# Kernel tuning notes

Hardware: AMD Instinct MI355X
Metric: run time of the kernel (lower is better)

## Reference

```python
import jax, jax.numpy as jnp
import numpy as np

N_FEAT = 1024
N_HIDDEN = 31


def _lstm_cell(x, h, c, W_ih, W_hh, b_ih, b_hh):
    # PyTorch LSTMCell: gates ordered i, f, g, o
    gates = x @ W_ih.T + b_ih + h @ W_hh.T + b_hh
    i, f, g, o = jnp.split(gates, 4, axis=-1)
    i = jax.nn.sigmoid(i)
    f = jax.nn.sigmoid(f)
    g = jnp.tanh(g)
    o = jax.nn.sigmoid(o)
    c_new = f * c + i * g
    h_new = o * jnp.tanh(c_new)
    return h_new, c_new


def setup_inputs() -> dict:
    key = jax.random.key(0)
    ks = jax.random.split(key, 12)
    B, T = 64, 512
    s1 = 1.0 / np.sqrt(N_HIDDEN)
    inp = {
        "input": jax.random.normal(ks[0], (B, T, N_FEAT), dtype=jnp.float32),
        "W_ih1": jax.random.uniform(ks[1], (4 * N_HIDDEN, N_FEAT), jnp.float32, -s1, s1),
        "W_hh1": jax.random.uniform(ks[2], (4 * N_HIDDEN, N_HIDDEN), jnp.float32, -s1, s1),
        "b_ih1": jax.random.uniform(ks[3], (4 * N_HIDDEN,), jnp.float32, -s1, s1),
        "b_hh1": jax.random.uniform(ks[4], (4 * N_HIDDEN,), jnp.float32, -s1, s1),
        "W_ih2": jax.random.uniform(ks[5], (4 * N_HIDDEN, N_HIDDEN), jnp.float32, -s1, s1),
        "W_hh2": jax.random.uniform(ks[6], (4 * N_HIDDEN, N_HIDDEN), jnp.float32, -s1, s1),
        "b_ih2": jax.random.uniform(ks[7], (4 * N_HIDDEN,), jnp.float32, -s1, s1),
        "b_hh2": jax.random.uniform(ks[8], (4 * N_HIDDEN,), jnp.float32, -s1, s1),
        "W_lin": jax.random.uniform(ks[9], (N_FEAT, N_HIDDEN), jnp.float32, -s1, s1),
        "b_lin": jax.random.uniform(ks[10], (N_FEAT,), jnp.float32, -s1, s1),
        "future": 16,
    }
    return inp


def reference(input, W_ih1, W_hh1, b_ih1, b_hh1, W_ih2, W_hh2, b_ih2, b_hh2, W_lin, b_lin, future):
    B = input.shape[0]
    h0 = jnp.zeros((B, N_HIDDEN), dtype=input.dtype)
    state0 = (h0, h0, h0, h0)  # h_t, c_t, h_t2, c_t2

    def step(state, x_t):
        h_t, c_t, h_t2, c_t2 = state
        h_t, c_t = _lstm_cell(x_t, h_t, c_t, W_ih1, W_hh1, b_ih1, b_hh1)
        h_t2, c_t2 = _lstm_cell(h_t, h_t2, c_t2, W_ih2, W_hh2, b_ih2, b_hh2)
        out = h_t2 @ W_lin.T + b_lin  # [B, N_FEAT]
        return (h_t, c_t, h_t2, c_t2), out

    # teacher-forced pass over the given sequence
    xs = jnp.swapaxes(input, 0, 1)  # [T, B, F]
    state, outs = jax.lax.scan(step, state0, xs)
    last = outs[-1]

    def fut_step(carry, _):
        state, out = carry
        state, out = step(state, out)
        return (state, out), out

    if future > 0:
        _, fut_outs = jax.lax.scan(fut_step, (state, last), None, length=future)
        outs = jnp.concatenate([outs, fut_outs], axis=0)

    return jnp.swapaxes(outs, 0, 1)  # [B, T+future, N_FEAT]
```

## Files before the change

kernel.cpp:

```cpp
#include <hip/hip_runtime.h>
#include <hip/hip_bf16.h>

#define BB_  64
#define TT_  512
#define FF_  1024
#define HH_  31
#define GG_  124
#define FUT_ 16
#define TTOT_ 528
#define OUT_ROW_ ((size_t)TTOT_ * FF_)

#define PRE1_OFF ((size_t)0)
#define H2A_OFF  (PRE1_OFF + (size_t)TT_*64*128)
#define WT_OFF   (H2A_OFF  + (size_t)TTOT_*64*32)
#define MV_OFF   (WT_OFF   + 31*1024)

__device__ __forceinline__ float rdlane(float v, int k) {
    return __uint_as_float(__builtin_amdgcn_readlane(__float_as_uint(v), k));
}

#define REP31(M) M(0) M(1) M(2) M(3) M(4) M(5) M(6) M(7) M(8) M(9) \
                 M(10) M(11) M(12) M(13) M(14) M(15) M(16) M(17) M(18) M(19) \
                 M(20) M(21) M(22) M(23) M(24) M(25) M(26) M(27) M(28) M(29) M(30)

__global__ void k0_prep(const float* __restrict__ Wlin, float* __restrict__ WT) {
    int i = blockIdx.x * 256 + threadIdx.x;
    int j = i / 31;
    int k = i - j * 31;
    WT[k * 1024 + j] = Wlin[i];
}

__global__ __launch_bounds__(64) void k0b_mv(
    const float* __restrict__ Wih1, const float* __restrict__ Wlin,
    const float* __restrict__ blin, float* __restrict__ Mv)
{
    int i = blockIdx.x * 64 + threadIdx.x;
    int g = i >> 5, k = i & 31;
    const float* wr = Wih1 + (size_t)g * FF_;
    float acc = 0.0f;
    if (k < 31) {
#pragma unroll 8
        for (int j = 0; j < FF_; j++) acc += wr[j] * Wlin[j * 31 + k];
    } else {
#pragma unroll 8
        for (int j = 0; j < FF_; j++) acc += wr[j] * blin[j];
    }
    Mv[i] = acc;
}

__global__ __launch_bounds__(256) void k1_pregate(
    const float* __restrict__ X,
    const float* __restrict__ Wih1,
    const float* __restrict__ bih1,
    const float* __restrict__ bhh1,
    float* __restrict__ pre1)
{
    __shared__ __align__(16) float xs[32][64];
    __shared__ __align__(16) float ws[32][128];
    const int tid  = threadIdx.x;
    const int t    = blockIdx.x;
    const int tcol = tid & 31, trow = tid >> 5;
    const int c0 = tcol * 4, r0 = trow * 8;

    float4 acc[8];
#pragma unroll
    for (int r = 0; r < 8; r++) acc[r] = make_float4(0.f, 0.f, 0.f, 0.f);

    for (int kc = 0; kc < 32; ++kc) {
        const int k0 = kc * 32;
#pragma unroll
        for (int p = 0; p < 2; p++) {
            int i = tid + p * 256;
            int r = i >> 3, f = i & 7;
            float4 v = *(const float4*)(X + (size_t)r * TT_ * FF_ + (size_t)t * FF_ + k0 + f * 4);
            xs[f * 4 + 0][r] = v.x; xs[f * 4 + 1][r] = v.y;
            xs[f * 4 + 2][r] = v.z; xs[f * 4 + 3][r] = v.w;
        }
#pragma unroll
        for (int p = 0; p < 4; p++) {
            int i = tid + p * 256;
            int g = i >> 3, f = i & 7;
            float4 v = make_float4(0.f, 0.f, 0.f, 0.f);
            if (g < GG_) v = *(const float4*)(Wih1 + (size_t)g * FF_ + k0 + f * 4);
            ws[f * 4 + 0][g] = v.x; ws[f * 4 + 1][g] = v.y;
            ws[f * 4 + 2][g] = v.z; ws[f * 4 + 3][g] = v.w;
        }
        __syncthreads();
#pragma unroll
        for (int k = 0; k < 32; k++) {
            float4 wv = *(const float4*)&ws[k][c0];
            float4 xa = *(const float4*)&xs[k][r0];
            float4 xb = *(const float4*)&xs[k][r0 + 4];
            float rx[8] = {xa.x, xa.y, xa.z, xa.w, xb.x, xb.y, xb.z, xb.w};
#pragma unroll
            for (int r = 0; r < 8; r++) {
                acc[r].x += rx[r] * wv.x; acc[r].y += rx[r] * wv.y;
                acc[r].z += rx[r] * wv.z; acc[r].w += rx[r] * wv.w;
            }
        }
        __syncthreads();
    }
    float bias[4];
#pragma unroll
    for (int cc = 0; cc < 4; cc++) {
        int c = c0 + cc;
        bias[cc] = (c < GG_) ? (bih1[c] + bhh1[c]) : 0.0f;
    }
#pragma unroll
    for (int r = 0; r < 8; r++) {
        int m = t * 64 + r0 + r;
        float4 o = acc[r];
        o.x += bias[0]; o.y += bias[1]; o.z += bias[2]; o.w += bias[3];
        *(float4*)(pre1 + (size_t)m * 128 + c0) = o;
    }
}

__global__ __attribute__((amdgpu_flat_work_group_size(128, 128), amdgpu_waves_per_eu(1)))
void k2_recur(
    const float* __restrict__ pre1,
    const float* __restrict__ Whh1,
    const float* __restrict__ Wih2,
    const float* __restrict__ Whh2,
    const float* __restrict__ bih1, const float* __restrict__ bhh1,
    const float* __restrict__ bih2, const float* __restrict__ bhh2,
    const float* __restrict__ Mv,
    float* __restrict__ h2a)
{
    __shared__ float gA[2][128];
    __shared__ float g2[2][128];
    const int L  = threadIdx.x;
    const int bb = blockIdx.x;
    const int j  = L & 63;
    const int gc = (L < GG_) ? L : (GG_ - 1);
    const bool isg = (gc >= 62 && gc < 93);
    const bool own = (j < HH_);

#define WLOAD(k) float w1_##k  = Whh1[gc * 31 + k]; \
                 float wi2_##k = Wih2[gc * 31 + k]; \
                 float wh2_##k = Whh2[gc * 31 + k];
    REP31(WLOAD)
#undef WLOAD
#define WPIN(k) asm("" : "+v"(w1_##k), "+v"(wi2_##k), "+v"(wh2_##k));
    REP31(WPIN)
#undef WPIN

    const float b2c = bih2[gc] + bhh2[gc];

    float hv1 = 0.0f, cv1 = 0.0f, hv2 = 0.0f, cv2 = 0.0f;

    float cur0 = pre1[(size_t)bb * 128 + L];
    float pnxt = pre1[((size_t)1 * 64 + bb) * 128 + L];
    {
        float a = cur0;
#define DOTP(k) { float hk = rdlane(hv1, k); a += w1_##k * hk; }
        REP31(DOTP)
#undef DOTP
        float z = isg ? (2.0f * a) : a;
        float s = 1.0f / (1.0f + __expf(-z));
        gA[1][L] = isg ? (2.0f * s - 1.0f) : s;
    }
    __syncthreads();
    if (own) {
        float ig = gA[1][j];
        float fg = gA[1][j + 31];
        float gg = gA[1][j + 62];
        float og = gA[1][j + 93];
        cv1 = fg * cv1 + ig * gg;
        float e = __expf(-2.0f * cv1);
        hv1 = og * (2.0f / (1.0f + e) - 1.0f);
    }

    for (int t = 0; t < TT_ - 1; t++) {
        const int pb = t & 1;
        const float cur = pnxt;
        float pld = 0.0f;
        if (t + 2 < TT_) pld = pre1[((size_t)(t + 2) * 64 + bb) * 128 + L];

        float b = b2c;
        float a = cur;
#define DOTM(k) { float h1k = rdlane(hv1, k); float h2k = rdlane(hv2, k); \
                  b += wi2_##k * h1k + wh2_##k * h2k; \
                  a += w1_##k * h1k; }
        REP31(DOTM)
#undef DOTM
        {
            float z = isg ? (2.0f * b) : b;
            float s = 1.0f / (1.0f + __expf(-z));
            g2[pb][L] = isg ? (2.0f * s - 1.0f) : s;
        }
        {
            float z = isg ? (2.0f * a) : a;
            float s = 1.0f / (1.0f + __expf(-z));
            gA[pb][L] = isg ? (2.0f * s - 1.0f) : s;
        }
        __syncthreads();
        if (own) {
            float ig = g2[pb][j];
            float fg = g2[pb][j + 31];
            float gg = g2[pb][j + 62];
            float og = g2[pb][j + 93];
            cv2 = fg * cv2 + ig * gg;
            float e = __expf(-2.0f * cv2);
            hv2 = og * (2.0f / (1.0f + e) - 1.0f);
            float i1 = gA[pb][j];
            float f1 = gA[pb][j + 31];
            float g1v = gA[pb][j + 62];
            float o1 = gA[pb][j + 93];
            cv1 = f1 * cv1 + i1 * g1v;
            float e1 = __expf(-2.0f * cv1);
            hv1 = o1 * (2.0f / (1.0f + e1) - 1.0f);
        }
        if (L < HH_) h2a[((size_t)t * 64 + bb) * 32 + L] = hv2;
        pnxt = pld;
    }

    {
        float b = b2c;
#define DOTT(k) { float h1k = rdlane(hv1, k); float h2k = rdlane(hv2, k); \
                  b += wi2_##k * h1k + wh2_##k * h2k; }
        REP31(DOTT)
#undef DOTT
        float z = isg ? (2.0f * b) : b;
        float s = 1.0f / (1.0f + __expf(-z));
        g2[1][L] = isg ? (2.0f * s - 1.0f) : s;
    }
    __syncthreads();
    if (own) {
        float ig = g2[1][j];
        float fg = g2[1][j + 31];
        float gg = g2[1][j + 62];
        float og = g2[1][j + 93];
        cv2 = fg * cv2 + ig * gg;
        float e = __expf(-2.0f * cv2);
        hv2 = og * (2.0f / (1.0f + e) - 1.0f);
    }
    if (L < HH_) h2a[((size_t)(TT_ - 1) * 64 + bb) * 32 + L] = hv2;

#define MLOAD(k) float m_##k = Mv[gc * 32 + k];
    REP31(MLOAD)
#undef MLOAD
    float m_31 = Mv[gc * 32 + 31];
#define MPIN(k) asm("" : "+v"(m_##k));
    REP31(MPIN)
#undef MPIN
    asm("" : "+v"(m_31));
    const float b1c = bih1[gc] + bhh1[gc];

    for (int sft = 0; sft < FUT_; sft++) {
        float a = b1c + m_31;
#define DOTF1(k) { float h2k = rdlane(hv2, k); a += m_##k * h2k; }
        REP31(DOTF1)
#undef DOTF1
#define DOTF2(k) { float hk = rdlane(hv1, k); a += w1_##k * hk; }
        REP31(DOTF2)
#undef DOTF2
        {
            float z = isg ? (2.0f * a) : a;
            float s = 1.0f / (1.0f + __expf(-z));
            gA[0][L] = isg ? (2.0f * s - 1.0f) : s;
        }
        __syncthreads();
        if (own) {
            float ig = gA[0][j];
            float fg = gA[0][j + 31];
            float gg = gA[0][j + 62];
            float og = gA[0][j + 93];
            cv1 = fg * cv1 + ig * gg;
            float e = __expf(-2.0f * cv1);
            hv1 = og * (2.0f / (1.0f + e) - 1.0f);
        }
        float b = b2c;
#define DOTF3(k) { float h1k = rdlane(hv1, k); float h2k = rdlane(hv2, k); \
                   b += wi2_##k * h1k + wh2_##k * h2k; }
        REP31(DOTF3)
#undef DOTF3
        {
            float z = isg ? (2.0f * b) : b;
            float s = 1.0f / (1.0f + __expf(-z));
            g2[0][L] = isg ? (2.0f * s - 1.0f) : s;
        }
        __syncthreads();
        if (own) {
            float ig = g2[0][j];
            float fg = g2[0][j + 31];
            float gg = g2[0][j + 62];
            float og = g2[0][j + 93];
            cv2 = fg * cv2 + ig * gg;
            float e = __expf(-2.0f * cv2);
            hv2 = og * (2.0f / (1.0f + e) - 1.0f);
        }
        if (L < HH_) h2a[((size_t)(TT_ + sft) * 64 + bb) * 32 + L] = hv2;
    }
}

__global__ __launch_bounds__(256) void k3_outlin(
    const float* __restrict__ h2a,
    const float* __restrict__ WT,
    const float* __restrict__ blin,
    float* __restrict__ out)
{
    __shared__ __align__(16) float hl[16][32];
    const int tid = threadIdx.x;
    const int m0  = blockIdx.x * 16;
#pragma unroll
    for (int p = 0; p < 2; p++) {
        int i = tid + p * 256;
        int r = i >> 5, k = i & 31;
        hl[r][k] = h2a[(size_t)(m0 + r) * 32 + k];
    }
    __syncthreads();
    const int c0 = tid * 4;
    float4 bl = *(const float4*)(blin + c0);
    float4 acc[16];
#pragma unroll
    for (int r = 0; r < 16; r++) acc[r] = bl;
    for (int k = 0; k < 31; k++) {
        float4 wv = *(const float4*)(WT + k * 1024 + c0);
#pragma unroll
        for (int r = 0; r < 16; r++) {
            float h = hl[r][k];
            acc[r].x += h * wv.x; acc[r].y += h * wv.y;
            acc[r].z += h * wv.z; acc[r].w += h * wv.w;
        }
    }
    const int t  = m0 >> 6;
    const int b0 = m0 & 63;
#pragma unroll
    for (int r = 0; r < 16; r++) {
        int b = b0 + r;
        *(float4*)(out + (size_t)b * OUT_ROW_ + (size_t)t * FF_ + c0) = acc[r];
    }
}

extern "C" void kernel_launch(void* const* d_in, const int* in_sizes, int n_in,
                              void* d_out, int out_size, void* d_ws, size_t ws_size,
                              hipStream_t stream) {
    (void)in_sizes; (void)n_in; (void)out_size; (void)ws_size;
    const float* X    = (const float*)d_in[0];
    const float* Wih1 = (const float*)d_in[1];
    const float* Whh1 = (const float*)d_in[2];
    const float* bih1 = (const float*)d_in[3];
    const float* bhh1 = (const float*)d_in[4];
    const float* Wih2 = (const float*)d_in[5];
    const float* Whh2 = (const float*)d_in[6];
    const float* bih2 = (const float*)d_in[7];
    const float* bhh2 = (const float*)d_in[8];
    const float* Wlin = (const float*)d_in[9];
    const float* blin = (const float*)d_in[10];

    float* ws   = (float*)d_ws;
    float* pre1 = ws + PRE1_OFF;
    float* h2a  = ws + H2A_OFF;
    float* WT   = ws + WT_OFF;
    float* Mv   = ws + MV_OFF;
    float* out  = (float*)d_out;

    hipLaunchKernelGGL(k0_prep,    dim3(124),  dim3(256), 0, stream, Wlin, WT);
    hipLaunchKernelGGL(k0b_mv,     dim3(62),   dim3(64),  0, stream, Wih1, Wlin, blin, Mv);
    hipLaunchKernelGGL(k1_pregate, dim3(TT_),  dim3(256), 0, stream, X, Wih1, bih1, bhh1, pre1);
    hipLaunchKernelGGL(k2_recur,   dim3(BB_),  dim3(128), 0, stream, pre1, Whh1, Wih2, Whh2,
                       bih1, bhh1, bih2, bhh2, Mv, h2a);
    hipLaunchKernelGGL(k3_outlin,  dim3(TTOT_*4), dim3(256), 0, stream, h2a, WT, blin, out);
}
```

Baseline: 834.9 us.

## Pack both LSTM layer states into one register and split dot-product accumulators

Layer-2 state now lives in lanes 0-31 and layer-1 state in lanes 32-63 of a single hv/cv register pair, so the two cell updates after each barrier run as one select-based path instead of two serial ones. Each dot product is split into even/odd partial accumulators to shorten the dependent FMA chain on the serial critical path. The pre1 prefetch is also moved one step further ahead. This trades some lane-select logic and extra registers for lower latency per timestep in a latency-bound recurrent kernel.

Result: faster. 809.9 us (-3.0%).

```diff
diff --git a/kernel.cpp b/kernel.cpp
--- a/kernel.cpp
+++ b/kernel.cpp
@@ -22,6 +22,10 @@
 #define REP31(M) M(0) M(1) M(2) M(3) M(4) M(5) M(6) M(7) M(8) M(9) \
                  M(10) M(11) M(12) M(13) M(14) M(15) M(16) M(17) M(18) M(19) \
                  M(20) M(21) M(22) M(23) M(24) M(25) M(26) M(27) M(28) M(29) M(30)
+#define REP16E(M) M(0) M(2) M(4) M(6) M(8) M(10) M(12) M(14) \
+                  M(16) M(18) M(20) M(22) M(24) M(26) M(28) M(30)
+#define REP15O(M) M(1) M(3) M(5) M(7) M(9) M(11) M(13) M(15) \
+                  M(17) M(19) M(21) M(23) M(25) M(27) M(29)
 
 __global__ void k0_prep(const float* __restrict__ Wlin, float* __restrict__ WT) {
     int i = blockIdx.x * 256 + threadIdx.x;
@@ -133,7 +137,8 @@
     const int j  = L & 63;
     const int gc = (L < GG_) ? L : (GG_ - 1);
     const bool isg = (gc >= 62 && gc < 93);
-    const bool own = (j < HH_);
+    const bool selhi = (j >= 32);
+    const int sidx = selhi ? (j - 32) : j;
 
 #define WLOAD(k) float w1_##k  = Whh1[gc * 31 + k]; \
                  float wi2_##k = Wih2[gc * 31 + k]; \
@@ -146,43 +151,56 @@
 
     const float b2c = bih2[gc] + bhh2[gc];
 
-    float hv1 = 0.0f, cv1 = 0.0f, hv2 = 0.0f, cv2 = 0.0f;
+    float hv = 0.0f, cv = 0.0f;
 
     float cur0 = pre1[(size_t)bb * 128 + L];
     float pnxt = pre1[((size_t)1 * 64 + bb) * 128 + L];
+    float pnx2 = pre1[((size_t)2 * 64 + bb) * 128 + L];
     {
-        float a = cur0;
-#define DOTP(k) { float hk = rdlane(hv1, k); a += w1_##k * hk; }
-        REP31(DOTP)
-#undef DOTP
+        float pa0 = cur0, pa1 = 0.0f;
+#define DPE(k) { float hk = rdlane(hv, 32 + k); pa0 += w1_##k * hk; }
+#define DPO(k) { float hk = rdlane(hv, 32 + k); pa1 += w1_##k * hk; }
+        REP16E(DPE)
+        REP15O(DPO)
+#undef DPE
+#undef DPO
+        float a = pa0 + pa1;
         float z = isg ? (2.0f * a) : a;
         float s = 1.0f / (1.0f + __expf(-z));
         gA[1][L] = isg ? (2.0f * s - 1.0f) : s;
     }
     __syncthreads();
-    if (own) {
-        float ig = gA[1][j];
-        float fg = gA[1][j + 31];
-        float gg = gA[1][j + 62];
-        float og = gA[1][j + 93];
-        cv1 = fg * cv1 + ig * gg;
-        float e = __expf(-2.0f * cv1);
-        hv1 = og * (2.0f / (1.0f + e) - 1.0f);
+    {
+        const float* gsrc = &gA[1][0];
+        float ig = gsrc[sidx];
+        float fg = gsrc[sidx + 31];
+        float gg = gsrc[sidx + 62];
+        float og = gsrc[sidx + 93];
+        float cvn = fg * cv + ig * gg;
+        float e = __expf(-2.0f * cvn);
+        float hvn = og * (2.0f / (1.0f + e) - 1.0f);
+        cv = selhi ? cvn : 0.0f;
+        hv = selhi ? hvn : 0.0f;
     }
 
     for (int t = 0; t < TT_ - 1; t++) {
         const int pb = t & 1;
         const float cur = pnxt;
-        float pld = 0.0f;
-        if (t + 2 < TT_) pld = pre1[((size_t)(t + 2) * 64 + bb) * 128 + L];
-
-        float b = b2c;
-        float a = cur;
-#define DOTM(k) { float h1k = rdlane(hv1, k); float h2k = rdlane(hv2, k); \
-                  b += wi2_##k * h1k + wh2_##k * h2k; \
-                  a += w1_##k * h1k; }
-        REP31(DOTM)
-#undef DOTM
+        pnxt = pnx2;
+        if (t + 3 < TT_) pnx2 = pre1[((size_t)(t + 3) * 64 + bb) * 128 + L];
+
+        float bi0 = b2c, bi1 = 0.0f, bh0 = 0.0f, bh1 = 0.0f;
+        float pa0 = cur, pa1 = 0.0f;
+#define DME(k) { float h1k = rdlane(hv, 32 + k); float h2k = rdlane(hv, k); \
+                 bi0 += wi2_##k * h1k; bh0 += wh2_##k * h2k; pa0 += w1_##k * h1k; }
+#define DMO(k) { float h1k = rdlane(hv, 32 + k); float h2k = rdlane(hv, k); \
+                 bi1 += wi2_##k * h1k; bh1 += wh2_##k * h2k; pa1 += w1_##k * h1k; }
+        REP16E(DME)
+        REP15O(DMO)
+#undef DME
+#undef DMO
+        float b = (bi0 + bi1) + (bh0 + bh1);
+        float a = pa0 + pa1;
         {
             float z = isg ? (2.0f * b) : b;
             float s = 1.0f / (1.0f + __expf(-z));
@@ -194,47 +212,48 @@
             gA[pb][L] = isg ? (2.0f * s - 1.0f) : s;
         }
         __syncthreads();
-        if (own) {
-            float ig = g2[pb][j];
-            float fg = g2[pb][j + 31];
-            float gg = g2[pb][j + 62];
-            float og = g2[pb][j + 93];
-            cv2 = fg * cv2 + ig * gg;
-            float e = __expf(-2.0f * cv2);
-            hv2 = og * (2.0f / (1.0f + e) - 1.0f);
-            float i1 = gA[pb][j];
-            float f1 = gA[pb][j + 31];
-            float g1v = gA[pb][j + 62];
-            float o1 = gA[pb][j + 93];
-            cv1 = f1 * cv1 + i1 * g1v;
-            float e1 = __expf(-2.0f * cv1);
-            hv1 = o1 * (2.0f / (1.0f + e1) - 1.0f);
-        }
-        if (L < HH_) h2a[((size_t)t * 64 + bb) * 32 + L] = hv2;
-        pnxt = pld;
+        {
+            const float* gsrc = selhi ? &gA[pb][0] : &g2[pb][0];
+            float ig = gsrc[sidx];
+            float fg = gsrc[sidx + 31];
+            float gg = gsrc[sidx + 62];
+            float og = gsrc[sidx + 93];
+            cv = fg * cv + ig * gg;
+            float e = __expf(-2.0f * cv);
+            hv = og * (2.0f / (1.0f + e) - 1.0f);
+        }
+        if (L < HH_) h2a[((size_t)t * 64 + bb) * 32 + L] = hv;
     }
 
     {
-        float b = b2c;
-#define DOTT(k) { float h1k = rdlane(hv1, k); float h2k = rdlane(hv2, k); \
-                  b += wi2_##k * h1k + wh2_##k * h2k; }
-        REP31(DOTT)
-#undef DOTT
+        float bi0 = b2c, bi1 = 0.0f, bh0 = 0.0f, bh1 = 0.0f;
+#define DTE(k) { float h1k = rdlane(hv, 32 + k); float h2k = rdlane(hv, k); \
+                 bi0 += wi2_##k * h1k; bh0 += wh2_##k * h2k; }
+#define DTO(k) { float h1k = rdlane(hv, 32 + k); float h2k = rdlane(hv, k); \
+                 bi1 += wi2_##k * h1k; bh1 += wh2_##k * h2k; }
+        REP16E(DTE)
+        REP15O(DTO)
+#undef DTE
+#undef DTO
+        float b = (bi0 + bi1) + (bh0 + bh1);
         float z = isg ? (2.0f * b) : b;
         float s = 1.0f / (1.0f + __expf(-z));
         g2[1][L] = isg ? (2.0f * s - 1.0f) : s;
     }
     __syncthreads();
-    if (own) {
-        float ig = g2[1][j];
-        float fg = g2[1][j + 31];
-        float gg = g2[1][j + 62];
-        float og = g2[1][j + 93];
-        cv2 = fg * cv2 + ig * gg;
-        float e = __expf(-2.0f * cv2);
-        hv2 = og * (2.0f / (1.0f + e) - 1.0f);
-    }
-    if (L < HH_) h2a[((size_t)(TT_ - 1) * 64 + bb) * 32 + L] = hv2;
+    {
+        const float* gsrc = &g2[1][0];
+        float ig = gsrc[sidx];
+        float fg = gsrc[sidx + 31];
+        float gg = gsrc[sidx + 62];
+        float og = gsrc[sidx + 93];
+        float cvn = fg * cv + ig * gg;
+        float e = __expf(-2.0f * cvn);
+        float hvn = og * (2.0f / (1.0f + e) - 1.0f);
+        cv = selhi ? cv : cvn;
+        hv = selhi ? hv : hvn;
+    }
+    if (L < HH_) h2a[((size_t)(TT_ - 1) * 64 + bb) * 32 + L] = hv;
 
 #define MLOAD(k) float m_##k = Mv[gc * 32 + k];
     REP31(MLOAD)
@@ -247,49 +266,67 @@
     const float b1c = bih1[gc] + bhh1[gc];
 
     for (int sft = 0; sft < FUT_; sft++) {
-        float a = b1c + m_31;
-#define DOTF1(k) { float h2k = rdlane(hv2, k); a += m_##k * h2k; }
-        REP31(DOTF1)
-#undef DOTF1
-#define DOTF2(k) { float hk = rdlane(hv1, k); a += w1_##k * hk; }
-        REP31(DOTF2)
-#undef DOTF2
-        {
+        float pa0 = b1c + m_31, pa1 = 0.0f;
+#define DFE(k) { float h2k = rdlane(hv, k); pa0 += m_##k * h2k; }
+#define DFO(k) { float h2k = rdlane(hv, k); pa1 += m_##k * h2k; }
+        REP16E(DFE)
+        REP15O(DFO)
+#undef DFE
+#undef DFO
+#define DGE(k) { float h1k = rdlane(hv, 32 + k); pa0 += w1_##k * h1k; }
+#define DGO(k) { float h1k = rdlane(hv, 32 + k); pa1 += w1_##k * h1k; }
+        REP16E(DGE)
+        REP15O(DGO)
+#undef DGE
+#undef DGO
+        {
+            float a = pa0 + pa1;
             float z = isg ? (2.0f * a) : a;
             float s = 1.0f / (1.0f + __expf(-z));
             gA[0][L] = isg ? (2.0f * s - 1.0f) : s;
         }
         __syncthreads();
-        if (own) {
-            float ig = gA[0][j];
-            float fg = gA[0][j + 31];
-            float gg = gA[0][j + 62];
-            float og = gA[0][j + 93];
-            cv1 = fg * cv1 + ig * gg;
-            float e = __expf(-2.0f * cv1);
-            hv1 = og * (2.0f / (1.0f + e) - 1.0f);
-        }
-        float b = b2c;
-#define DOTF3(k) { float h1k = rdlane(hv1, k); float h2k = rdlane(hv2, k); \
-                   b += wi2_##k * h1k + wh2_##k * h2k; }
-        REP31(DOTF3)
-#undef DOTF3
-        {
+        {
+            const float* gsrc = &gA[0][0];
+            float ig = gsrc[sidx];
+            float fg = gsrc[sidx + 31];
+            float gg = gsrc[sidx + 62];
+            float og = gsrc[sidx + 93];
+            float cvn = fg * cv + ig * gg;
+            float e = __expf(-2.0f * cvn);
+            float hvn = og * (2.0f / (1.0f + e) - 1.0f);
+            cv = selhi ? cvn : cv;
+            hv = selhi ? hvn : hv;
+        }
+        float bi0 = b2c, bi1 = 0.0f, bh0 = 0.0f, bh1 = 0.0f;
+#define DHE(k) { float h1k = rdlane(hv, 32 + k); float h2k = rdlane(hv, k); \
+                 bi0 += wi2_##k * h1k; bh0 += wh2_##k * h2k; }
+#define DHO(k) { float h1k = rdlane(hv, 32 + k); float h2k = rdlane(hv, k); \
+                 bi1 += wi2_##k * h1k; bh1 += wh2_##k * h2k; }
+        REP16E(DHE)
+        REP15O(DHO)
+#undef DHE
+#undef DHO
+        {
+            float b = (bi0 + bi1) + (bh0 + bh1);
             float z = isg ? (2.0f * b) : b;
             float s = 1.0f / (1.0f + __expf(-z));
             g2[0][L] = isg ? (2.0f * s - 1.0f) : s;
         }
         __syncthreads();
-        if (own) {
-            float ig = g2[0][j];
-            float fg = g2[0][j + 31];
-            float gg = g2[0][j + 62];
-            float og = g2[0][j + 93];
-            cv2 = fg * cv2 + ig * gg;
-            float e = __expf(-2.0f * cv2);
-            hv2 = og * (2.0f / (1.0f + e) - 1.0f);
-        }
-        if (L < HH_) h2a[((size_t)(TT_ + sft) * 64 + bb) * 32 + L] = hv2;
+        {
+            const float* gsrc = &g2[0][0];
+            float ig = gsrc[sidx];
+            float fg = gsrc[sidx + 31];
+            float gg = gsrc[sidx + 62];
+            float og = gsrc[sidx + 93];
+            float cvn = fg * cv + ig * gg;
+            float e = __expf(-2.0f * cvn);
+            float hvn = og * (2.0f / (1.0f + e) - 1.0f);
+            cv = selhi ? cv : cvn;
+            hv = selhi ? hv : hvn;
+        }
+        if (L < HH_) h2a[((size_t)(TT_ + sft) * 64 + bb) * 32 + L] = hv;
     }
 }
 
```
